# Kernel optimization log

Measured on AMD Instinct MI355X. Metric: run time of the kernel, lower is better.

Reference implementation:

```python
import jax, jax.numpy as jnp
import numpy as np

TEMPERATURE = 30.0


def _adaptive_pool_28(sk):
    # sk: [b, 1, H, W] with H, W divisible by 28 -> [b, 1, 28, 28]
    b, c, h, w = sk.shape
    fh, fw = h // 28, w // 28
    return sk.reshape(b, c, 28, fh, 28, fw).mean(axis=(3, 5))


def setup_inputs() -> dict:
    key = jax.random.key(0)
    ks = jax.random.split(key, 6)
    bs, C, H, W, K = 8, 256, 64, 64, 16
    return {
        "x": jax.random.normal(ks[0], (bs, C, H, W), dtype=jnp.float32),
        "scene_knowledge": jax.random.normal(ks[1], (bs, 1, 56, 56), dtype=jnp.float32),
        "weight": jax.random.normal(ks[2], (K, C, C, 3, 3), dtype=jnp.float32) * 0.02,
        "bias": jax.random.normal(ks[3], (K, C), dtype=jnp.float32) * 0.02,
        "att_w1": jax.random.normal(ks[4], (196, 784), dtype=jnp.float32) * 0.05,
        "att_w2": jax.random.normal(ks[5], (16, 196), dtype=jnp.float32) * 0.05,
    }


def reference(x, scene_knowledge, weight, bias, att_w1, att_w2):
    bs, C, h, w = x.shape
    K = weight.shape[0]

    # ---- Attention: pooled scene knowledge -> softmax over K experts ----
    pooled = _adaptive_pool_28(scene_knowledge).reshape(bs, 28 * 28)  # [bs, 784]
    hdn = jax.nn.relu(pooled @ att_w1.T)                               # [bs, 196]
    logits = hdn @ att_w2.T                                            # [bs, K]
    att = jax.nn.softmax(logits / TEMPERATURE, axis=-1)                # [bs, K]

    # ---- Aggregate per-sample conv weights and biases ----
    agg_w = jnp.einsum("bk,koihw->boihw", att, weight)  # [bs, C, C, 3, 3]
    agg_b = att @ bias                                   # [bs, C]

    # ---- Per-sample conv (equivalent to groups=bs trick in torch) ----
    def per_sample_conv(xi, wi):
        # xi: [C, h, w], wi: [C, C, 3, 3]
        return jax.lax.conv_general_dilated(
            xi[None], wi, window_strides=(1, 1), padding="SAME",
            dimension_numbers=("NCHW", "OIHW", "NCHW"))[0]

    out = jax.vmap(per_sample_conv)(x, agg_w)            # [bs, C, h, w]
    out = out + agg_b[:, :, None, None] + x              # bias + residual
    return out
```

## Files before the change

kernel.cpp:

```cpp
#include <hip/hip_runtime.h>
#include <stdint.h>
#include <stddef.h>

typedef __bf16 bf16;
typedef __bf16 bf16x8 __attribute__((ext_vector_type(8)));
typedef __bf16 bf16x4 __attribute__((ext_vector_type(4)));
typedef float f32x4 __attribute__((ext_vector_type(4)));

static_assert(sizeof(bf16x8) == 16, "bf16x8 must be 16B");

__device__ __forceinline__ void gload_lds16(const void* g, void* l) {
    __builtin_amdgcn_global_load_lds(
        (const __attribute__((address_space(1))) uint32_t*)g,
        (__attribute__((address_space(3))) uint32_t*)l, 16, 0, 0);
}

__global__ __launch_bounds__(1024) void attn_kernel(const float* __restrict__ sk,
                                                    const float* __restrict__ w1,
                                                    const float* __restrict__ w2,
                                                    float* __restrict__ att) {
    const int b = blockIdx.x, t = threadIdx.x;
    __shared__ float pooled[784];
    __shared__ float hdn[196];
    __shared__ float logits[16];
    const float* skb = sk + (size_t)b * 3136;
    if (t < 784) {
        int oy = t / 28, ox = t % 28;
        const float* p = skb + (oy * 2) * 56 + ox * 2;
        pooled[t] = 0.25f * (p[0] + p[1] + p[56] + p[57]);
    }
    __syncthreads();
    const int q = t & 15, jg = t >> 4;
#pragma unroll
    for (int rep = 0; rep < 4; ++rep) {
        const int j = rep * 64 + jg;
        float s = 0.f;
        if (j < 196) {
            const float* wr = w1 + (size_t)j * 784 + q;
#pragma unroll 7
            for (int i = 0; i < 49; ++i) s += pooled[q + i * 16] * wr[i * 16];
        }
#pragma unroll
        for (int off = 8; off; off >>= 1) s += __shfl_xor(s, off, 16);
        if (j < 196 && q == 0) hdn[j] = s > 0.f ? s : 0.f;
    }
    __syncthreads();
    if (t < 256) {
        const int jj = t >> 4, qq = t & 15;
        float s = 0.f;
#pragma unroll
        for (int i = 0; i < 13; ++i) {
            const int idx = qq + i * 16;
            if (idx < 196) s += hdn[idx] * w2[jj * 196 + idx];
        }
#pragma unroll
        for (int off = 8; off; off >>= 1) s += __shfl_xor(s, off, 16);
        if (qq == 0) logits[jj] = s * (1.0f / 30.0f);
    }
    __syncthreads();
    if (t == 0) {
        float m = logits[0];
        for (int k = 1; k < 16; ++k) m = fmaxf(m, logits[k]);
        float e16[16], sum = 0.f;
        for (int k = 0; k < 16; ++k) { e16[k] = expf(logits[k] - m); sum += e16[k]; }
        float inv = 1.f / sum;
        for (int k = 0; k < 16; ++k) att[b * 16 + k] = e16[k] * inv;
    }
}

__global__ __launch_bounds__(256) void agg_kernel(
    const float* __restrict__ weight,
    const float* __restrict__ bias,
    const float* __restrict__ att,
    bf16* __restrict__ aggw,
    float* __restrict__ aggb) {
    const int bid = blockIdx.x;
    const int co = bid & 255, chunk = bid >> 8;
    const int t = threadIdx.x;

    __shared__ bf16 accW[8 * 576];

    if (chunk == 0 && t < 8) {
        float s = 0.f;
        for (int k = 0; k < 16; ++k) s += att[t * 16 + k] * bias[k * 256 + co];
        aggb[t * 256 + co] = s;
    }

    if (t < 144) {
        const float* wbase = weight + (size_t)co * 2304 + (size_t)chunk * 576 + (size_t)t * 4;
        float4 wv[16];
#pragma unroll
        for (int k = 0; k < 16; ++k)
            wv[k] = *(const float4*)(wbase + (size_t)k * 589824);
        float a[8][4];
#pragma unroll
        for (int b = 0; b < 8; ++b)
#pragma unroll
            for (int j = 0; j < 4; ++j) a[b][j] = 0.f;
#pragma unroll
        for (int k = 0; k < 16; ++k) {
#pragma unroll
            for (int b = 0; b < 8; ++b) {
                const float av = att[b * 16 + k];
                a[b][0] += av * wv[k].x;
                a[b][1] += av * wv[k].y;
                a[b][2] += av * wv[k].z;
                a[b][3] += av * wv[k].w;
            }
        }
#pragma unroll
        for (int b = 0; b < 8; ++b) {
            bf16x4 v;
#pragma unroll
            for (int j = 0; j < 4; ++j) v[j] = (bf16)a[b][j];
            *(bf16x4*)&accW[b * 576 + t * 4] = v;
        }
    }
    __syncthreads();

    const int half = co >> 7, co_l = co & 127;
    for (int s = t; s < 576; s += 256) {
        const int b = s / 72, r = s - b * 72;
        const int pos = r >> 3, cg = r & 7;
        bf16x8 v;
#pragma unroll
        for (int c = 0; c < 8; ++c) v[c] = accW[b * 576 + (cg * 8 + c) * 9 + pos];
        size_t o = (((((size_t)b * 9 + pos) * 4 + chunk) * 2 + half) * 8 + cg) * 128 + co_l;
        *(bf16x8*)(aggw + o * 8) = v;
    }
}

__global__ void transpose_kernel(const float* __restrict__ x, bf16* __restrict__ xt) {
    const int bid = blockIdx.x;
    const int b = bid >> 6, y = bid & 63;
    const int t = threadIdx.x;
    __shared__ bf16 T[256 * 64];
    const float* src = x + (size_t)b * 256 * 4096 + (size_t)y * 64;
    for (int i = 0; i < 16; ++i) {
        int v = t + 256 * i;
        int ci = v >> 4, x4 = (v & 15) * 4;
        float4 f = *(const float4*)(src + (size_t)ci * 4096 + x4);
        bf16* d = &T[ci * 64 + x4];
        d[0] = (bf16)f.x; d[1] = (bf16)f.y; d[2] = (bf16)f.z; d[3] = (bf16)f.w;
    }
    __syncthreads();
    bf16* dstb = xt + (size_t)bid * 16384;
    for (int i = 0; i < 8; ++i) {
        int c2 = t + 256 * i;
        int cg = c2 >> 6, xx = c2 & 63;
        bf16x8 v;
#pragma unroll
        for (int c = 0; c < 8; ++c) v[c] = T[(cg * 8 + c) * 64 + xx];
        *(bf16x8*)(dstb + (size_t)c2 * 8) = v;
    }
}

__global__ __launch_bounds__(256, 2) void conv_kernel(
    const bf16* __restrict__ xt, const bf16* __restrict__ aggw,
    const float* __restrict__ aggb, const float* __restrict__ xin,
    float* __restrict__ out) {
    const int bid = blockIdx.x;
    const int slice = bid & 15, ytile = bid >> 4;
    const int b = slice >> 1, half = slice & 1;
    const int tid = threadIdx.x;
    const int wave = tid >> 6, lane = tid & 63;
    const int wm = wave & 1, wn = wave >> 1;
    const int lane15 = lane & 15, quad = lane >> 4;

    __shared__ __align__(16) bf16 Xs[4][8][66][8];

    f32x4 acc[4][4];
#pragma unroll
    for (int mt = 0; mt < 4; ++mt)
#pragma unroll
        for (int nt = 0; nt < 4; ++nt) acc[mt][nt] = f32x4{0.f, 0.f, 0.f, 0.f};

    {
        uint4 z; z.x = z.y = z.z = z.w = 0u;
        uint4* p = (uint4*)&Xs[0][0][0][0];
        for (int i = tid; i < 2112; i += 256) p[i] = z;
    }
    __syncthreads();

    const int yrow = ytile * 2 - 1 + wave;
    const bool rowok = (yrow >= 0) && (yrow < 64);
    const bf16* xsrc = xt + ((size_t)b * 64 + (rowok ? yrow : 0)) * 16384 + (size_t)lane * 8;
    bf16* xdstbase = &Xs[wave][0][1][0];

    const bf16* wlane = aggw + (size_t)b * 589824 + (size_t)half * 8192
                      + (size_t)quad * 1024 + (size_t)(wm * 64 + lane15) * 8;

    bf16x8 afr[2][2][4];

    if (rowok) {
#pragma unroll
        for (int cg = 0; cg < 8; ++cg)
            gload_lds16(xsrc + cg * 512, xdstbase + cg * 528);
    }
#pragma unroll
    for (int s_ = 0; s_ < 2; ++s_)
#pragma unroll
        for (int mt = 0; mt < 4; ++mt)
            afr[0][s_][mt] = *(const bf16x8*)(wlane + s_ * 4096 + mt * 128);
    asm volatile("s_waitcnt vmcnt(0)" ::: "memory");
    __builtin_amdgcn_s_barrier();

    for (int cp = 0; cp < 2; ++cp) {
#pragma unroll
        for (int t = 0; t < 18; ++t) {
            const int par = t & 1;
            const int pos = t % 9;
            const int chunk = cp * 2 + t / 9;
            if (t < 17) {
                const int npos = (t + 1) % 9;
                const int nchunk = cp * 2 + (t + 1) / 9;
                const bf16* pb = wlane + (size_t)npos * 65536 + (size_t)nchunk * 16384;
#pragma unroll
                for (int s_ = 0; s_ < 2; ++s_)
#pragma unroll
                    for (int mt = 0; mt < 4; ++mt)
                        afr[par ^ 1][s_][mt] = *(const bf16x8*)(pb + s_ * 4096 + mt * 128);
            } else if (cp == 0) {
                const bf16* pb = wlane + (size_t)(cp * 2 + 2) * 16384;
#pragma unroll
                for (int s_ = 0; s_ < 2; ++s_)
#pragma unroll
                    for (int mt = 0; mt < 4; ++mt)
                        afr[par ^ 1][s_][mt] = *(const bf16x8*)(pb + s_ * 4096 + mt * 128);
            }
            const int kh = pos / 3, kw = pos - kh * 3;
            const int xr = wn + kh;
#pragma unroll
            for (int s_ = 0; s_ < 2; ++s_) {
                const int cg = s_ * 4 + quad;
                bf16x8 bfr[4];
#pragma unroll
                for (int nt = 0; nt < 4; ++nt)
                    bfr[nt] = *(const bf16x8*)&Xs[xr][cg][kw + nt * 16 + lane15][0];
#pragma unroll
                for (int mt = 0; mt < 4; ++mt)
#pragma unroll
                    for (int nt = 0; nt < 4; ++nt)
                        acc[mt][nt] = __builtin_amdgcn_mfma_f32_16x16x32_bf16(
                            afr[par][s_][mt], bfr[nt], acc[mt][nt], 0, 0, 0);
            }
            if (pos == 8 && (t == 8 || cp == 0)) {
                asm volatile("s_waitcnt lgkmcnt(0)" ::: "memory");
                __builtin_amdgcn_s_barrier();
                if (rowok) {
                    const bf16* s0 = xsrc + (size_t)(chunk + 1) * 4096;
#pragma unroll
                    for (int cg = 0; cg < 8; ++cg)
                        gload_lds16(s0 + cg * 512, xdstbase + cg * 528);
                }
                asm volatile("s_waitcnt vmcnt(0)" ::: "memory");
                __builtin_amdgcn_s_barrier();
            }
        }
    }

    const int y = ytile * 2 + wn;
#pragma unroll
    for (int mt = 0; mt < 4; ++mt) {
#pragma unroll
        for (int r = 0; r < 4; ++r) {
            const int co = half * 128 + wm * 64 + mt * 16 + quad * 4 + r;
            const float bbv = aggb[b * 256 + co];
            const size_t rowbase = (((size_t)b * 256 + co) * 64 + y) * 64;
#pragma unroll
            for (int nt = 0; nt < 4; ++nt) {
                const size_t oidx = rowbase + nt * 16 + lane15;
                out[oidx] = acc[mt][nt][r] + bbv + xin[oidx];
            }
        }
    }
}

extern "C" void kernel_launch(void* const* d_in, const int* in_sizes, int n_in,
                              void* d_out, int out_size, void* d_ws, size_t ws_size,
                              hipStream_t stream) {
    const float* x    = (const float*)d_in[0];
    const float* sk   = (const float*)d_in[1];
    const float* wgt  = (const float*)d_in[2];
    const float* bias = (const float*)d_in[3];
    const float* w1   = (const float*)d_in[4];
    const float* w2   = (const float*)d_in[5];
    float* out = (float*)d_out;

    char* ws = (char*)d_ws;
    float* att  = (float*)(ws + 0);
    float* aggb = (float*)(ws + 1024);
    bf16*  aggw = (bf16*)(ws + 16384);
    bf16*  xt   = (bf16*)(ws + 16384 + 9437184);

    attn_kernel<<<8, 1024, 0, stream>>>(sk, w1, w2, att);
    agg_kernel<<<1024, 256, 0, stream>>>(wgt, bias, att, aggw, aggb);
    transpose_kernel<<<512, 256, 0, stream>>>(x, xt);
    conv_kernel<<<512, 256, 0, stream>>>(xt, aggw, aggb, x, out);
}
```

Baseline: 198.3 us.

## Stage conv weights in LDS with full 256-channel tiles and merge agg/transpose kernels

The conv kernel now computes all 256 output channels per block, so each block covers one batch and two rows and the grid halves to 256 blocks. Weights for each tap are double-buffered into LDS with global_load_lds instead of per-lane register loads, and the input is double-buffered as well. The aggregation and transpose kernels are merged into one launch. This cuts redundant input reads and one launch, but halves the block count to one per CU, doubles accumulator registers, and adds a barrier per tap.

```diff
diff --git a/kernel.cpp b/kernel.cpp
--- a/kernel.cpp
+++ b/kernel.cpp
@@ -68,17 +68,45 @@
     }
 }
 
-__global__ __launch_bounds__(256) void agg_kernel(
+__global__ __launch_bounds__(256) void aggt_kernel(
     const float* __restrict__ weight,
     const float* __restrict__ bias,
     const float* __restrict__ att,
     bf16* __restrict__ aggw,
-    float* __restrict__ aggb) {
+    float* __restrict__ aggb,
+    const float* __restrict__ x,
+    bf16* __restrict__ xt) {
+    __shared__ __align__(16) char smem[32768];
+    const int t = threadIdx.x;
+
+    if (blockIdx.x >= 1024) {
+        const int bid = blockIdx.x - 1024;
+        const int b = bid >> 6, y = bid & 63;
+        bf16* T = (bf16*)smem;
+        const float* src = x + (size_t)b * 256 * 4096 + (size_t)y * 64;
+        for (int i = 0; i < 16; ++i) {
+            int v = t + 256 * i;
+            int ci = v >> 4, x4 = (v & 15) * 4;
+            float4 f = *(const float4*)(src + (size_t)ci * 4096 + x4);
+            bf16* d = &T[ci * 64 + x4];
+            d[0] = (bf16)f.x; d[1] = (bf16)f.y; d[2] = (bf16)f.z; d[3] = (bf16)f.w;
+        }
+        __syncthreads();
+        bf16* dstb = xt + (size_t)bid * 16384;
+        for (int i = 0; i < 8; ++i) {
+            int c2 = t + 256 * i;
+            int cg = c2 >> 6, xx = c2 & 63;
+            bf16x8 v;
+#pragma unroll
+            for (int c = 0; c < 8; ++c) v[c] = T[(cg * 8 + c) * 64 + xx];
+            *(bf16x8*)(dstb + (size_t)c2 * 8) = v;
+        }
+        return;
+    }
+
     const int bid = blockIdx.x;
     const int co = bid & 255, chunk = bid >> 8;
-    const int t = threadIdx.x;
-
-    __shared__ bf16 accW[8 * 576];
+    bf16* accW = (bf16*)smem;
 
     if (chunk == 0 && t < 8) {
         float s = 0.f;
@@ -130,129 +158,98 @@
     }
 }
 
-__global__ void transpose_kernel(const float* __restrict__ x, bf16* __restrict__ xt) {
-    const int bid = blockIdx.x;
-    const int b = bid >> 6, y = bid & 63;
-    const int t = threadIdx.x;
-    __shared__ bf16 T[256 * 64];
-    const float* src = x + (size_t)b * 256 * 4096 + (size_t)y * 64;
-    for (int i = 0; i < 16; ++i) {
-        int v = t + 256 * i;
-        int ci = v >> 4, x4 = (v & 15) * 4;
-        float4 f = *(const float4*)(src + (size_t)ci * 4096 + x4);
-        bf16* d = &T[ci * 64 + x4];
-        d[0] = (bf16)f.x; d[1] = (bf16)f.y; d[2] = (bf16)f.z; d[3] = (bf16)f.w;
-    }
-    __syncthreads();
-    bf16* dstb = xt + (size_t)bid * 16384;
-    for (int i = 0; i < 8; ++i) {
-        int c2 = t + 256 * i;
-        int cg = c2 >> 6, xx = c2 & 63;
-        bf16x8 v;
-#pragma unroll
-        for (int c = 0; c < 8; ++c) v[c] = T[(cg * 8 + c) * 64 + xx];
-        *(bf16x8*)(dstb + (size_t)c2 * 8) = v;
-    }
-}
-
-__global__ __launch_bounds__(256, 2) void conv_kernel(
+__global__ __launch_bounds__(256, 1) void conv_kernel(
     const bf16* __restrict__ xt, const bf16* __restrict__ aggw,
     const float* __restrict__ aggb, const float* __restrict__ xin,
     float* __restrict__ out) {
     const int bid = blockIdx.x;
-    const int slice = bid & 15, ytile = bid >> 4;
-    const int b = slice >> 1, half = slice & 1;
+    const int b = bid & 7, ytile = bid >> 3;
     const int tid = threadIdx.x;
     const int wave = tid >> 6, lane = tid & 63;
     const int wm = wave & 1, wn = wave >> 1;
     const int lane15 = lane & 15, quad = lane >> 4;
 
-    __shared__ __align__(16) bf16 Xs[4][8][66][8];
-
-    f32x4 acc[4][4];
-#pragma unroll
-    for (int mt = 0; mt < 4; ++mt)
+    __shared__ __align__(16) bf16 Ws[2][16384];
+    __shared__ __align__(16) bf16 Xs[2][4][8][66][8];
+
+    f32x4 acc[8][4];
+#pragma unroll
+    for (int mt = 0; mt < 8; ++mt)
 #pragma unroll
         for (int nt = 0; nt < 4; ++nt) acc[mt][nt] = f32x4{0.f, 0.f, 0.f, 0.f};
 
     {
         uint4 z; z.x = z.y = z.z = z.w = 0u;
-        uint4* p = (uint4*)&Xs[0][0][0][0];
-        for (int i = tid; i < 2112; i += 256) p[i] = z;
+        uint4* p = (uint4*)&Xs[0][0][0][0][0];
+        for (int i = tid; i < 4224; i += 256) p[i] = z;
     }
     __syncthreads();
 
     const int yrow = ytile * 2 - 1 + wave;
     const bool rowok = (yrow >= 0) && (yrow < 64);
     const bf16* xsrc = xt + ((size_t)b * 64 + (rowok ? yrow : 0)) * 16384 + (size_t)lane * 8;
-    bf16* xdstbase = &Xs[wave][0][1][0];
-
-    const bf16* wlane = aggw + (size_t)b * 589824 + (size_t)half * 8192
-                      + (size_t)quad * 1024 + (size_t)(wm * 64 + lane15) * 8;
-
-    bf16x8 afr[2][2][4];
+    bf16* xdst0 = &Xs[0][wave][0][1][0];
+    bf16* xdst1 = &Xs[1][wave][0][1][0];
+
+    const bf16* wsrcw = aggw + (size_t)b * 589824 + (size_t)wave * 4096 + (size_t)lane * 8;
+    bf16* wdstw0 = &Ws[0][0] + wave * 4096;
+    bf16* wdstw1 = &Ws[1][0] + wave * 4096;
 
     if (rowok) {
 #pragma unroll
         for (int cg = 0; cg < 8; ++cg)
-            gload_lds16(xsrc + cg * 512, xdstbase + cg * 528);
-    }
-#pragma unroll
-    for (int s_ = 0; s_ < 2; ++s_)
-#pragma unroll
-        for (int mt = 0; mt < 4; ++mt)
-            afr[0][s_][mt] = *(const bf16x8*)(wlane + s_ * 4096 + mt * 128);
+            gload_lds16(xsrc + cg * 512, xdst0 + cg * 528);
+    }
+#pragma unroll
+    for (int i = 0; i < 8; ++i)
+        gload_lds16(wsrcw + i * 512, wdstw0 + i * 512);
     asm volatile("s_waitcnt vmcnt(0)" ::: "memory");
     __builtin_amdgcn_s_barrier();
 
-    for (int cp = 0; cp < 2; ++cp) {
-#pragma unroll
-        for (int t = 0; t < 18; ++t) {
-            const int par = t & 1;
-            const int pos = t % 9;
-            const int chunk = cp * 2 + t / 9;
-            if (t < 17) {
-                const int npos = (t + 1) % 9;
-                const int nchunk = cp * 2 + (t + 1) / 9;
-                const bf16* pb = wlane + (size_t)npos * 65536 + (size_t)nchunk * 16384;
-#pragma unroll
-                for (int s_ = 0; s_ < 2; ++s_)
-#pragma unroll
-                    for (int mt = 0; mt < 4; ++mt)
-                        afr[par ^ 1][s_][mt] = *(const bf16x8*)(pb + s_ * 4096 + mt * 128);
-            } else if (cp == 0) {
-                const bf16* pb = wlane + (size_t)(cp * 2 + 2) * 16384;
-#pragma unroll
-                for (int s_ = 0; s_ < 2; ++s_)
-#pragma unroll
-                    for (int mt = 0; mt < 4; ++mt)
-                        afr[par ^ 1][s_][mt] = *(const bf16x8*)(pb + s_ * 4096 + mt * 128);
-            }
-            const int kh = pos / 3, kw = pos - kh * 3;
+    for (int chunk = 0; chunk < 4; ++chunk) {
+        const bf16* xbase = (chunk & 1) ? &Xs[1][0][0][0][0] : &Xs[0][0][0][0][0];
+        for (int pos = 0; pos < 9; ++pos) {
+            const int t = chunk * 9 + pos;
+            const bf16* wcur = (t & 1) ? &Ws[1][0] : &Ws[0][0];
+            bf16* wnxt = (t & 1) ? wdstw0 : wdstw1;
+            if (t < 35) {
+                int npos = pos + 1, nchunk = chunk;
+                if (npos == 9) { npos = 0; nchunk = chunk + 1; }
+                const bf16* s0 = wsrcw + (size_t)(npos * 4 + nchunk) * 16384;
+#pragma unroll
+                for (int i = 0; i < 8; ++i)
+                    gload_lds16(s0 + i * 512, wnxt + i * 512);
+            }
+            if (pos == 8 && chunk < 3 && rowok) {
+                const bf16* s0 = xsrc + (size_t)(chunk + 1) * 4096;
+                bf16* xd = (chunk & 1) ? xdst0 : xdst1;
+#pragma unroll
+                for (int cg = 0; cg < 8; ++cg)
+                    gload_lds16(s0 + cg * 512, xd + cg * 528);
+            }
+            const int kh = (pos >= 6) ? 2 : (pos >= 3) ? 1 : 0;
+            const int kw = pos - kh * 3;
             const int xr = wn + kh;
+            const bf16* xrow = xbase + xr * 4224;
 #pragma unroll
             for (int s_ = 0; s_ < 2; ++s_) {
                 const int cg = s_ * 4 + quad;
-                bf16x8 bfr[4];
+                bf16x8 afr[8], bfr[4];
+#pragma unroll
+                for (int mt = 0; mt < 8; ++mt)
+                    afr[mt] = *(const bf16x8*)(wcur + wm * 8192 + cg * 1024
+                                               + (mt * 16 + lane15) * 8);
 #pragma unroll
                 for (int nt = 0; nt < 4; ++nt)
-                    bfr[nt] = *(const bf16x8*)&Xs[xr][cg][kw + nt * 16 + lane15][0];
-#pragma unroll
-                for (int mt = 0; mt < 4; ++mt)
+                    bfr[nt] = *(const bf16x8*)(xrow + cg * 528 + (kw + nt * 16 + lane15) * 8);
+#pragma unroll
+                for (int mt = 0; mt < 8; ++mt)
 #pragma unroll
                     for (int nt = 0; nt < 4; ++nt)
                         acc[mt][nt] = __builtin_amdgcn_mfma_f32_16x16x32_bf16(
-                            afr[par][s_][mt], bfr[nt], acc[mt][nt], 0, 0, 0);
-            }
-            if (pos == 8 && (t == 8 || cp == 0)) {
-                asm volatile("s_waitcnt lgkmcnt(0)" ::: "memory");
-                __builtin_amdgcn_s_barrier();
-                if (rowok) {
-                    const bf16* s0 = xsrc + (size_t)(chunk + 1) * 4096;
-#pragma unroll
-                    for (int cg = 0; cg < 8; ++cg)
-                        gload_lds16(s0 + cg * 512, xdstbase + cg * 528);
-                }
+                            afr[mt], bfr[nt], acc[mt][nt], 0, 0, 0);
+            }
+            if (t < 35) {
                 asm volatile("s_waitcnt vmcnt(0)" ::: "memory");
                 __builtin_amdgcn_s_barrier();
             }
@@ -261,10 +258,10 @@
 
     const int y = ytile * 2 + wn;
 #pragma unroll
-    for (int mt = 0; mt < 4; ++mt) {
+    for (int mt = 0; mt < 8; ++mt) {
 #pragma unroll
         for (int r = 0; r < 4; ++r) {
-            const int co = half * 128 + wm * 64 + mt * 16 + quad * 4 + r;
+            const int co = wm * 128 + mt * 16 + quad * 4 + r;
             const float bbv = aggb[b * 256 + co];
             const size_t rowbase = (((size_t)b * 256 + co) * 64 + y) * 64;
 #pragma unroll
@@ -294,7 +291,6 @@
     bf16*  xt   = (bf16*)(ws + 16384 + 9437184);
 
     attn_kernel<<<8, 1024, 0, stream>>>(sk, w1, w2, att);
-    agg_kernel<<<1024, 256, 0, stream>>>(wgt, bias, att, aggw, aggb);
-    transpose_kernel<<<512, 256, 0, stream>>>(x, xt);
-    conv_kernel<<<512, 256, 0, stream>>>(xt, aggw, aggb, x, out);
-}
+    aggt_kernel<<<1536, 256, 0, stream>>>(wgt, bias, att, aggw, aggb, x, xt);
+    conv_kernel<<<256, 256, 0, stream>>>(xt, aggw, aggb, x, out);
+}
```

Result: faster. 190.7 us (-3.8%).
